# Optimization experiments

Hardware: AMD Instinct MI355X
Metric: run time of the kernel (lower is better)

Reference implementation:

```python
import jax, jax.numpy as jnp
import numpy as np

ALPHA = 3.0      # sharpness in tanh(alpha * lin(x)) (HypergraphConstructor)
TOPK = 10        # scale_hyperedges: neighbors per node in similarity topk
NEG_SLOPE = 0.2  # LeakyReLU slope in HypergraphAttention


def setup_inputs() -> dict:
    key = jax.random.key(0)
    ks = jax.random.split(key, 8)
    B, L, N, F, D, E = 16, 64, 512, 64, 64, 40
    return {
        "x": jax.random.normal(ks[0], (B, L, N, F), jnp.float32),
        "idx": jnp.arange(N, dtype=jnp.int64) if jax.config.jax_enable_x64 else jnp.arange(N, dtype=jnp.int32),
        "emb1": 0.1 * jax.random.normal(ks[1], (N, E), jnp.float32),
        "lin1_w": jax.random.normal(ks[2], (E, E), jnp.float32) / np.float32(np.sqrt(E)),
        "lin1_b": jnp.zeros((E,), jnp.float32),
        "W_self": 0.1 * jax.random.normal(ks[3], (F, D), jnp.float32),
        "W_neigh": 0.1 * jax.random.normal(ks[4], (F, D), jnp.float32),
        "W_concat": 0.1 * jax.random.normal(ks[5], (2 * D, D), jnp.float32),
        "attention": 0.1 * jax.random.normal(ks[6], (2 * D, 1), jnp.float32),
    }


def build_incidence(idx, emb1, lin1_w, lin1_b):
    """HypergraphConstructor (similarity-topk branch). Returns H: (N_nodes, M_hyperedges)."""
    feats = jnp.tanh(ALPHA * (emb1[idx] @ lin1_w + lin1_b))        # (N, E)
    sim = feats @ feats.T                                          # (N, N)
    _, top = jax.lax.top_k(sim, TOPK)                              # (N, k) indices
    n = feats.shape[0]
    rows = jnp.arange(n)[:, None]
    H = jnp.zeros((n, n), feats.dtype).at[rows, top].set(1.0)      # row i = hyperedge from node i's neighbors
    return H.T                                                     # (N nodes, M hyperedges)


def hypergraph_attention(x, H, W_self, W_neigh, W_concat, attention):
    """Faithful HypergraphAttention.forward (eval mode: dropout is identity)."""
    x_self = jnp.einsum('blnf,fd->blnd', x, W_self)
    # aggregate nodes -> hyperedges: H.T[m,n] == H[n,m]
    he = jnp.einsum('nm,blnf->blmf', H, x)                          # (B, L, M, F)
    e_deg = jnp.maximum(H.sum(axis=0), 1.0)                        # (M,)
    he = he / e_deg[None, None, :, None]
    he = jnp.where(he >= 0, he, NEG_SLOPE * he)                    # LeakyReLU(0.2)
    # scatter hyperedges -> nodes
    x_neigh = jnp.einsum('nm,blmf->blnf', H, he)                   # (B, L, N, F)
    n_deg = jnp.maximum(H.sum(axis=1), 1.0)                        # (N,)
    x_neigh = x_neigh / n_deg[None, None, :, None]
    x_neigh = jnp.einsum('blnf,fd->blnd', x_neigh, W_neigh)
    x_cat = jnp.concatenate([x_self, x_neigh], axis=-1)            # (B, L, N, 2D)
    scores = jnp.squeeze(x_cat @ attention, axis=-1)               # (B, L, N)
    w = jax.nn.softmax(scores, axis=-1)                            # softmax over nodes
    return (x_cat * w[..., None]) @ W_concat                       # (B, L, N, D)


def reference(x, idx, emb1, lin1_w, lin1_b, W_self, W_neigh, W_concat, attention):
    H = build_incidence(idx, emb1, lin1_w, lin1_b)
    return hypergraph_attention(x, H, W_self, W_neigh, W_concat, attention)
```

## Files before the change

kernel.cpp:

```cpp
#include <hip/hip_runtime.h>

#define N_NODES 512
#define E_DIM   40
#define TOPK    10

typedef unsigned short u16;
typedef __attribute__((ext_vector_type(8))) short short8;
typedef __attribute__((ext_vector_type(4))) float f32x4;

__device__ __forceinline__ u16 f2bf(float f) {
    unsigned int b = __float_as_uint(f);
    b += 0x7fffu + ((b >> 16) & 1u);
    return (u16)(b >> 16);
}
__device__ __forceinline__ float bf2f(u16 u) {
    return __uint_as_float(((unsigned int)u) << 16);
}
__device__ __forceinline__ unsigned pk2(float a, float b) {
    return (unsigned)f2bf(a) | ((unsigned)f2bf(b) << 16);
}

__global__ void prep_kernel(const float* __restrict__ emb1,
                            const float* __restrict__ w,
                            const float* __restrict__ b,
                            float* __restrict__ feats,
                            const float* __restrict__ Ws, const float* __restrict__ Wn,
                            const float* __restrict__ Wc, const float* __restrict__ att,
                            u16* __restrict__ Wt, float* __restrict__ ap) {
    if (blockIdx.x < N_NODES) {
        int n = blockIdx.x, e = threadIdx.x;
        if (e >= E_DIM) return;
        const float* er = emb1 + n * E_DIM;
        float s = b[e];
        for (int k = 0; k < E_DIM; ++k) s += er[k] * w[k * E_DIM + e];
        feats[n * E_DIM + e] = tanhf(3.0f * s);
    } else {
        int f = blockIdx.x - N_NODES, d = threadIdx.x;
        float a = 0.f, bb = 0.f;
        for (int k = 0; k < 64; ++k) {
            a  += Ws[f * 64 + k] * Wc[k * 64 + d];
            bb += Wn[f * 64 + k] * Wc[(64 + k) * 64 + d];
        }
        Wt[d * 128 + f]      = f2bf(a);
        Wt[d * 128 + 64 + f] = f2bf(bb);
        float p0 = Ws[f * 64 + d] * att[d];
        float p1 = Wn[f * 64 + d] * att[64 + d];
        for (int off = 32; off > 0; off >>= 1) {
            p0 += __shfl_down(p0, off);
            p1 += __shfl_down(p1, off);
        }
        if (d == 0) { ap[f] = p0; ap[64 + f] = p1; }
    }
}

#define TOPK_SMEM (512 * 41 * 4 + 4 * 512 * 4)

__global__ __launch_bounds__(256) void topk_kernel(const float* __restrict__ feats,
                                                   u16* __restrict__ top16) {
    extern __shared__ float tsm[];
    float* sf   = tsm;
    float* ssim = tsm + 512 * 41;
    const int tid = threadIdx.x;
    for (int i = tid; i < 512 * E_DIM; i += 256) {
        int n = i / E_DIM, k = i - n * E_DIM;
        sf[n * 41 + k] = feats[i];
    }
    __syncthreads();
    const int wv = tid >> 6, lane = tid & 63;
    const int m = blockIdx.x * 4 + wv;
    float* sim = ssim + wv * 512;

    float fm[E_DIM];
#pragma unroll
    for (int k = 0; k < E_DIM; ++k) fm[k] = sf[m * 41 + k];
    for (int n = lane; n < N_NODES; n += 64) {
        const float* fr = &sf[n * 41];
        float s = 0.f;
#pragma unroll
        for (int k = 0; k < E_DIM; ++k) s += fm[k] * fr[k];
        sim[n] = s;
    }
    __syncthreads();
    for (int it = 0; it < TOPK; ++it) {
        float bv = -3.0e38f; int bi = 1 << 30;
        for (int n = lane; n < N_NODES; n += 64) {
            float v = sim[n];
            if (v > bv) { bv = v; bi = n; }
        }
        for (int off = 32; off > 0; off >>= 1) {
            float ov = __shfl_down(bv, off);
            int   oi = __shfl_down(bi, off);
            if (ov > bv || (ov == bv && oi < bi)) { bv = ov; bi = oi; }
        }
        bi = __shfl(bi, 0);
        if (lane == 0) top16[m * 16 + it] = (u16)bi;
        __syncthreads();
        sim[bi] = -3.0e38f;
        __syncthreads();
    }
}

__global__ void hbuild_kernel(const u16* __restrict__ top16,
                              u16* __restrict__ Hrow, u16* __restrict__ H,
                              int* __restrict__ deg) {
    int m = threadIdx.x;
#pragma unroll
    for (int j = 0; j < TOPK; ++j) {
        int n = (int)top16[m * 16 + j];
        Hrow[m * 512 + n] = 0x3F80;
        H[n * 512 + m]    = 0x3F80;
        atomicAdd(&deg[n], 1);
    }
}

#define SC_OFF  65536
#define RED_OFF 67584
#define SMEM_BYTES 67648

__device__ __forceinline__ int t64_byte(int f, int g) {
    return f * 1024 + ((g ^ (f & 7)) << 4);
}
__device__ __forceinline__ int rm_byte(int n, int g) {
    return n * 128 + ((g ^ (n & 7)) << 4);
}

__global__ __launch_bounds__(256, 2) void main_kernel(
    const float* __restrict__ x,
    const u16* __restrict__ Hrow, const u16* __restrict__ H,
    const int* __restrict__ deg,
    const u16* __restrict__ Wt, const float* __restrict__ ap,
    float* __restrict__ out)
{
    extern __shared__ char smem[];
    float* sc  = (float*)(smem + SC_OFF);
    float* red = (float*)(smem + RED_OFF);

    const int bl  = blockIdx.x;
    const int tid = threadIdx.x;
    const int wv = tid >> 6, lane = tid & 63;
    const int lrow = lane & 15, lk = lane >> 4;
    const float* xr   = x   + (size_t)bl * N_NODES * 64;
    float*       outr = out + (size_t)bl * N_NODES * 64;

    float sv2[2];
#pragma unroll
    for (int r = 0; r < 2; ++r) {
        const int row = tid + r * 256;
        const float4* px = (const float4*)(xr + row * 64);
        const int gcol = row >> 3, bcol = (row & 7) * 2;
        float s = 0.f;
#pragma unroll
        for (int g = 0; g < 8; ++g) {
            float4 v0 = px[2 * g], v1 = px[2 * g + 1];
            float4 a0 = *(const float4*)(ap + g * 8);
            float4 a1 = *(const float4*)(ap + g * 8 + 4);
            s += v0.x * a0.x + v0.y * a0.y + v0.z * a0.z + v0.w * a0.w
               + v1.x * a1.x + v1.y * a1.y + v1.z * a1.z + v1.w * a1.w;
            float vf[8] = { v0.x, v0.y, v0.z, v0.w, v1.x, v1.y, v1.z, v1.w };
#pragma unroll
            for (int j = 0; j < 8; ++j) {
                int f = g * 8 + j;
                *(u16*)(smem + t64_byte(f, gcol) + bcol) = f2bf(vf[j]);
            }
        }
        sv2[r] = s;
    }
    __syncthreads();

    {
        f32x4 acc[2][4][4];
#pragma unroll
        for (int h = 0; h < 2; ++h)
#pragma unroll
            for (int mt = 0; mt < 4; ++mt)
#pragma unroll
                for (int ft = 0; ft < 4; ++ft) acc[h][mt][ft] = (f32x4)0.f;
        for (int ks = 0; ks < 16; ++ks) {
            short8 bfr[4];
#pragma unroll
            for (int ft = 0; ft < 4; ++ft)
                bfr[ft] = *(const short8*)(smem + t64_byte(ft * 16 + lrow, ks * 4 + lk));
#pragma unroll
            for (int h = 0; h < 2; ++h) {
                const int wveff = wv + 4 * h;
                short8 afr[4];
#pragma unroll
                for (int mt = 0; mt < 4; ++mt)
                    afr[mt] = *(const short8*)(Hrow + (wveff * 64 + mt * 16 + lrow) * 512
                                                    + ks * 32 + lk * 8);
#pragma unroll
                for (int mt = 0; mt < 4; ++mt)
#pragma unroll
                    for (int ft = 0; ft < 4; ++ft)
                        acc[h][mt][ft] = __builtin_amdgcn_mfma_f32_16x16x32_bf16(
                            afr[mt], bfr[ft], acc[h][mt][ft], 0, 0, 0);
            }
        }
        __syncthreads();
#pragma unroll
        for (int h = 0; h < 2; ++h) {
            const int wveff = wv + 4 * h;
#pragma unroll
            for (int mt = 0; mt < 4; ++mt) {
                const int gm = wveff * 8 + mt * 2 + (lk >> 1);
#pragma unroll
                for (int ft = 0; ft < 4; ++ft) {
                    const int f = ft * 16 + lrow;
                    float v[4];
#pragma unroll
                    for (int r = 0; r < 4; ++r) {
                        float t = acc[h][mt][ft][r] * 0.1f;
                        v[r] = t >= 0.f ? t : 0.2f * t;
                    }
                    *(uint2*)(smem + t64_byte(f, gm) + (lk & 1) * 8) =
                        make_uint2(pk2(v[0], v[1]), pk2(v[2], v[3]));
                }
            }
        }
    }
    __syncthreads();

    {
        f32x4 acc[2][4][4];
#pragma unroll
        for (int h = 0; h < 2; ++h)
#pragma unroll
            for (int nt = 0; nt < 4; ++nt)
#pragma unroll
                for (int ft = 0; ft < 4; ++ft) acc[h][nt][ft] = (f32x4)0.f;
        for (int ks = 0; ks < 16; ++ks) {
            short8 afr[4];
#pragma unroll
            for (int ft = 0; ft < 4; ++ft)
                afr[ft] = *(const short8*)(smem + t64_byte(ft * 16 + lrow, ks * 4 + lk));
#pragma unroll
            for (int h = 0; h < 2; ++h) {
                const int wveff = wv + 4 * h;
                short8 bfr[4];
#pragma unroll
                for (int nt = 0; nt < 4; ++nt)
                    bfr[nt] = *(const short8*)(H + (wveff * 64 + nt * 16 + lrow) * 512
                                                 + ks * 32 + lk * 8);
#pragma unroll
                for (int nt = 0; nt < 4; ++nt)
#pragma unroll
                    for (int ft = 0; ft < 4; ++ft)
                        acc[h][nt][ft] = __builtin_amdgcn_mfma_f32_16x16x32_bf16(
                            afr[ft], bfr[nt], acc[h][nt][ft], 0, 0, 0);
            }
        }
        __syncthreads();
#pragma unroll
        for (int h = 0; h < 2; ++h) {
#pragma unroll
            for (int nt = 0; nt < 4; ++nt) {
                const int n = (wv + 4 * h) * 64 + nt * 16 + lrow;
                int dg = deg[n];
                const float ideg = 1.0f / (float)(dg > 0 ? dg : 1);
#pragma unroll
                for (int ft = 0; ft < 4; ++ft) {
                    const int gf = ft * 2 + (lk >> 1);
                    *(uint2*)(smem + rm_byte(n, gf) + (lk & 1) * 8) =
                        make_uint2(pk2(acc[h][nt][ft][0] * ideg, acc[h][nt][ft][1] * ideg),
                                   pk2(acc[h][nt][ft][2] * ideg, acc[h][nt][ft][3] * ideg));
                }
            }
        }
    }
    __syncthreads();

#pragma unroll
    for (int r = 0; r < 2; ++r) {
        const int row = tid + r * 256;
        float s = sv2[r];
#pragma unroll
        for (int g = 0; g < 8; ++g) {
            short8 q = *(const short8*)(smem + rm_byte(row, g));
            float4 b0 = *(const float4*)(ap + 64 + g * 8);
            float4 b1 = *(const float4*)(ap + 64 + g * 8 + 4);
            s += bf2f((u16)q[0]) * b0.x + bf2f((u16)q[1]) * b0.y
               + bf2f((u16)q[2]) * b0.z + bf2f((u16)q[3]) * b0.w
               + bf2f((u16)q[4]) * b1.x + bf2f((u16)q[5]) * b1.y
               + bf2f((u16)q[6]) * b1.z + bf2f((u16)q[7]) * b1.w;
        }
        sv2[r] = s;
    }
    float bv = fmaxf(sv2[0], sv2[1]);
#pragma unroll
    for (int off = 32; off > 0; off >>= 1) bv = fmaxf(bv, __shfl_xor(bv, off));
    if (lane == 0) red[wv] = bv;
    __syncthreads();
    float M = fmaxf(fmaxf(red[0], red[1]), fmaxf(red[2], red[3]));
    float e0 = expf(sv2[0] - M), e1 = expf(sv2[1] - M);
    sc[tid] = e0;
    sc[tid + 256] = e1;
    float sv = e0 + e1;
#pragma unroll
    for (int off = 32; off > 0; off >>= 1) sv += __shfl_xor(sv, off);
    if (lane == 0) red[4 + wv] = sv;
    __syncthreads();
    const float invS = 1.0f / (red[4] + red[5] + red[6] + red[7]);

#pragma unroll 1
    for (int h = 0; h < 2; ++h) {
        const int wveff = wv + 4 * h;
        for (int nt = 0; nt < 4; ++nt) {
            const int n = wveff * 64 + nt * 16 + lrow;
            f32x4 accn[4];
#pragma unroll
            for (int dt = 0; dt < 4; ++dt) accn[dt] = (f32x4)0.f;
#pragma unroll
            for (int ks = 0; ks < 4; ++ks) {
                short8 bfrag;
                if (ks < 2) {
                    const float4* px = (const float4*)(xr + n * 64 + ks * 32 + lk * 8);
                    float4 v0 = px[0], v1 = px[1];
                    union { uint4 u; short8 s8; } cv;
                    cv.u.x = pk2(v0.x, v0.y); cv.u.y = pk2(v0.z, v0.w);
                    cv.u.z = pk2(v1.x, v1.y); cv.u.w = pk2(v1.z, v1.w);
                    bfrag = cv.s8;
                } else {
                    int gx = (ks - 2) * 4 + lk;
                    bfrag = *(const short8*)(smem + rm_byte(n, gx));
                }
#pragma unroll
                for (int dt = 0; dt < 4; ++dt) {
                    short8 wfrag = *(const short8*)(Wt + (dt * 16 + lrow) * 128
                                                       + ks * 32 + lk * 8);
                    accn[dt] = __builtin_amdgcn_mfma_f32_16x16x32_bf16(
                        wfrag, bfrag, accn[dt], 0, 0, 0);
                }
            }
            const float ww = sc[n] * invS;
#pragma unroll
            for (int dt = 0; dt < 4; ++dt) {
                float4 f;
                f.x = accn[dt][0] * ww; f.y = accn[dt][1] * ww;
                f.z = accn[dt][2] * ww; f.w = accn[dt][3] * ww;
                *(float4*)(outr + n * 64 + dt * 16 + lk * 4) = f;
            }
        }
    }
}

#define WS_FEATS 0
#define WS_TOP   81920
#define WS_WT    98304
#define WS_AP    114688
#define WS_DEG   115200
#define WS_HROW  131072
#define WS_H     655360
#define WS_END   1179648

extern "C" void kernel_launch(void* const* d_in, const int* in_sizes, int n_in,
                              void* d_out, int out_size, void* d_ws, size_t ws_size,
                              hipStream_t stream) {
    const float* x        = (const float*)d_in[0];
    const float* emb1     = (const float*)d_in[2];
    const float* lin1_w   = (const float*)d_in[3];
    const float* lin1_b   = (const float*)d_in[4];
    const float* W_self   = (const float*)d_in[5];
    const float* W_neigh  = (const float*)d_in[6];
    const float* W_concat = (const float*)d_in[7];
    const float* att      = (const float*)d_in[8];
    float* out = (float*)d_out;

    char* ws = (char*)d_ws;
    float* feats = (float*)(ws + WS_FEATS);
    u16*   top16 = (u16*)  (ws + WS_TOP);
    u16*   Wt    = (u16*)  (ws + WS_WT);
    float* ap    = (float*)(ws + WS_AP);
    int*   deg   = (int*)  (ws + WS_DEG);
    u16*   Hrow  = (u16*)  (ws + WS_HROW);
    u16*   H     = (u16*)  (ws + WS_H);

    prep_kernel<<<N_NODES + 64, 64, 0, stream>>>(emb1, lin1_w, lin1_b, feats,
                                                 W_self, W_neigh, W_concat, att, Wt, ap);

    (void)hipFuncSetAttribute((const void*)topk_kernel,
                              hipFuncAttributeMaxDynamicSharedMemorySize, TOPK_SMEM);
    topk_kernel<<<128, 256, TOPK_SMEM, stream>>>(feats, top16);

    (void)hipMemsetAsync(ws + WS_DEG, 0, WS_END - WS_DEG, stream);
    hbuild_kernel<<<1, 512, 0, stream>>>(top16, Hrow, H, deg);

    (void)hipFuncSetAttribute((const void*)main_kernel,
                              hipFuncAttributeMaxDynamicSharedMemorySize, SMEM_BYTES);
    main_kernel<<<1024, 256, SMEM_BYTES, stream>>>(x, Hrow, H, deg, Wt, ap, out);
}
```

Before: 229.4 us.

## Split fused main kernel into hyperedge, softmax and output kernels for more parallelism

Replaces the single per-slice fused kernel with three kernels when the workspace is large enough. A hyperedge kernel computes the bf16 hyperedge features over 4096 blocks, and the attention term is folded algebraically so softmax scores come from x·a_self plus H·(he·a) per node. A separate softmax kernel computes the weights, and an output kernel over 2048 blocks does the scatter and final projection. This buys more blocks and higher occupancy (3 blocks per CU) at the cost of a 64MB heT round trip through memory plus extra launches. It also hardcodes the edge degree as 0.1, i.e. 1/TOPK, and uses atomics for hv.

```diff
diff --git a/kernel.cpp b/kernel.cpp
--- a/kernel.cpp
+++ b/kernel.cpp
@@ -113,15 +113,282 @@
     }
 }
 
+
+#define HE_SMEM 32832
+__device__ __forceinline__ int t32_byte(int f, int g) {
+    return f * 1024 + ((g ^ (f & 7)) << 4);
+}
+
+__global__ __launch_bounds__(256, 3) void he_kernel(
+    const float* __restrict__ x, const u16* __restrict__ Hrow,
+    const float* __restrict__ ap,
+    u16* __restrict__ heT, float* __restrict__ hv)
+{
+    extern __shared__ char smem[];
+    const int bid = blockIdx.x;
+    const int slice = bid >> 2, mhalf = (bid >> 1) & 1, fhalf = bid & 1;
+    const int tid = threadIdx.x;
+    const int wv = tid >> 6, lane = tid & 63;
+    const int lrow = lane & 15, lk = lane >> 4;
+    const float* xr = x + (size_t)slice * N_NODES * 64;
+    const int mbase = mhalf * 256 + wv * 64;
+
+#pragma unroll
+    for (int r = 0; r < 2; ++r) {
+        const int row = tid + r * 256;
+        const float4* px = (const float4*)(xr + row * 64 + fhalf * 32);
+        const int gcol = row >> 3, bcol = (row & 7) * 2;
+#pragma unroll
+        for (int g = 0; g < 4; ++g) {
+            float4 v0 = px[2 * g], v1 = px[2 * g + 1];
+            float vf[8] = { v0.x, v0.y, v0.z, v0.w, v1.x, v1.y, v1.z, v1.w };
+#pragma unroll
+            for (int j = 0; j < 8; ++j) {
+                int f = g * 8 + j;
+                *(u16*)(smem + t32_byte(f, gcol) + bcol) = f2bf(vf[j]);
+            }
+        }
+    }
+    __syncthreads();
+
+    f32x4 acc[4][2];
+#pragma unroll
+    for (int mt = 0; mt < 4; ++mt)
+#pragma unroll
+        for (int fh = 0; fh < 2; ++fh) acc[mt][fh] = (f32x4)0.f;
+    for (int ks = 0; ks < 16; ++ks) {
+        short8 afr[4], bfr[2];
+#pragma unroll
+        for (int mt = 0; mt < 4; ++mt)
+            afr[mt] = *(const short8*)(Hrow + (mbase + mt * 16 + lrow) * 512
+                                            + ks * 32 + lk * 8);
+#pragma unroll
+        for (int fh = 0; fh < 2; ++fh)
+            bfr[fh] = *(const short8*)(smem + t32_byte(fh * 16 + lrow, ks * 4 + lk));
+#pragma unroll
+        for (int mt = 0; mt < 4; ++mt)
+#pragma unroll
+            for (int fh = 0; fh < 2; ++fh)
+                acc[mt][fh] = __builtin_amdgcn_mfma_f32_16x16x32_bf16(
+                    afr[mt], bfr[fh], acc[mt][fh], 0, 0, 0);
+    }
+
+    float lv[4][2][4];
+#pragma unroll
+    for (int mt = 0; mt < 4; ++mt)
+#pragma unroll
+        for (int fh = 0; fh < 2; ++fh)
+#pragma unroll
+            for (int r = 0; r < 4; ++r) {
+                float t = acc[mt][fh][r] * 0.1f;
+                lv[mt][fh][r] = t >= 0.f ? t : 0.2f * t;
+            }
+
+#pragma unroll
+    for (int mt = 0; mt < 4; ++mt)
+#pragma unroll
+        for (int r = 0; r < 4; ++r) {
+            float p = lv[mt][0][r] * ap[64 + fhalf * 32 + lrow]
+                    + lv[mt][1][r] * ap[64 + fhalf * 32 + 16 + lrow];
+            p += __shfl_xor(p, 1);
+            p += __shfl_xor(p, 2);
+            p += __shfl_xor(p, 4);
+            p += __shfl_xor(p, 8);
+            if (lrow == 0)
+                atomicAdd(&hv[slice * 512 + mbase + mt * 16 + lk * 4 + r], p);
+        }
+    __syncthreads();
+
+#pragma unroll
+    for (int mt = 0; mt < 4; ++mt)
+#pragma unroll
+        for (int fh = 0; fh < 2; ++fh)
+#pragma unroll
+            for (int r = 0; r < 4; ++r) {
+                int f_l = fh * 16 + lrow;
+                int m_l = mt * 16 + lk * 4 + r;
+                *(u16*)(smem + wv * 4096 + f_l * 128
+                        + (((m_l >> 3) ^ (f_l & 7)) << 4) + (m_l & 7) * 2)
+                    = f2bf(lv[mt][fh][r]);
+            }
+    __syncthreads();
+
+    {
+        const int f_l = lane & 31, gb = (lane >> 5) * 4;
+#pragma unroll
+        for (int gi = 0; gi < 4; ++gi) {
+            int g = gb + gi;
+            uint4 v = *(const uint4*)(smem + wv * 4096 + f_l * 128
+                                      + ((g ^ (f_l & 7)) << 4));
+            *(uint4*)(heT + (size_t)slice * 32768 + (fhalf * 32 + f_l) * 512
+                      + mbase + g * 8) = v;
+        }
+    }
+}
+
+__global__ __launch_bounds__(512) void sm_kernel(
+    const float* __restrict__ x, const u16* __restrict__ H,
+    const int* __restrict__ deg, const float* __restrict__ ap,
+    const float* __restrict__ hv, float* __restrict__ wexp)
+{
+    __shared__ float hvl[512];
+    __shared__ float red[16];
+    const int slice = blockIdx.x, n = threadIdx.x;
+    const int wv = n >> 6, lane = n & 63;
+    hvl[n] = hv[slice * 512 + n];
+    __syncthreads();
+
+    const float4* px = (const float4*)(x + (size_t)slice * N_NODES * 64 + n * 64);
+    float s = 0.f;
+#pragma unroll
+    for (int g = 0; g < 8; ++g) {
+        float4 v0 = px[2 * g], v1 = px[2 * g + 1];
+        float4 a0 = *(const float4*)(ap + g * 8);
+        float4 a1 = *(const float4*)(ap + g * 8 + 4);
+        s += v0.x * a0.x + v0.y * a0.y + v0.z * a0.z + v0.w * a0.w
+           + v1.x * a1.x + v1.y * a1.y + v1.z * a1.z + v1.w * a1.w;
+    }
+    const uint4* hp = (const uint4*)(H + n * 512);
+    float t = 0.f;
+    for (int c = 0; c < 64; ++c) {
+        uint4 h = hp[c];
+        unsigned wd[4] = { h.x, h.y, h.z, h.w };
+#pragma unroll
+        for (int p = 0; p < 4; ++p) {
+            t += bf2f((u16)(wd[p] & 0xffff))  * hvl[c * 8 + p * 2];
+            t += bf2f((u16)(wd[p] >> 16))     * hvl[c * 8 + p * 2 + 1];
+        }
+    }
+    int dg = deg[n];
+    s += t * (1.0f / (float)(dg > 0 ? dg : 1));
+
+    float bv = s;
+#pragma unroll
+    for (int off = 32; off > 0; off >>= 1) bv = fmaxf(bv, __shfl_xor(bv, off));
+    if (lane == 0) red[wv] = bv;
+    __syncthreads();
+    float M = red[0];
+#pragma unroll
+    for (int w = 1; w < 8; ++w) M = fmaxf(M, red[w]);
+    float ev = expf(s - M);
+    float sv = ev;
+#pragma unroll
+    for (int off = 32; off > 0; off >>= 1) sv += __shfl_xor(sv, off);
+    if (lane == 0) red[8 + wv] = sv;
+    __syncthreads();
+    float S = red[8];
+#pragma unroll
+    for (int w = 1; w < 8; ++w) S += red[8 + w];
+    wexp[slice * 512 + n] = ev * (1.0f / S);
+}
+
+#define OUT_SMEM 32832
+__device__ __forceinline__ int rm_byte(int nl, int g) {
+    return nl * 128 + ((g ^ (nl & 7)) << 4);
+}
+
+__global__ __launch_bounds__(256, 3) void out_kernel(
+    const float* __restrict__ x, const u16* __restrict__ H,
+    const int* __restrict__ deg, const u16* __restrict__ heT,
+    const u16* __restrict__ Wt, const float* __restrict__ wexp,
+    float* __restrict__ out)
+{
+    extern __shared__ char smem[];
+    const int bid = blockIdx.x;
+    const int slice = bid >> 1, nhalf = bid & 1;
+    const int tid = threadIdx.x;
+    const int wv = tid >> 6, lane = tid & 63;
+    const int lrow = lane & 15, lk = lane >> 4;
+    const float* xr   = x   + (size_t)slice * N_NODES * 64;
+    float*       outr = out + (size_t)slice * N_NODES * 64;
+    const u16* heTs = heT + (size_t)slice * 32768;
+    const int nbase = nhalf * 256 + wv * 64;
+
+    {
+        f32x4 acc[4][4];
+#pragma unroll
+        for (int nt = 0; nt < 4; ++nt)
+#pragma unroll
+            for (int ft = 0; ft < 4; ++ft) acc[nt][ft] = (f32x4)0.f;
+        for (int ks = 0; ks < 16; ++ks) {
+            short8 afr[4], bfr[4];
+#pragma unroll
+            for (int ft = 0; ft < 4; ++ft)
+                afr[ft] = *(const short8*)(heTs + (ft * 16 + lrow) * 512
+                                                + ks * 32 + lk * 8);
+#pragma unroll
+            for (int nt = 0; nt < 4; ++nt)
+                bfr[nt] = *(const short8*)(H + (nbase + nt * 16 + lrow) * 512
+                                             + ks * 32 + lk * 8);
+#pragma unroll
+            for (int nt = 0; nt < 4; ++nt)
+#pragma unroll
+                for (int ft = 0; ft < 4; ++ft)
+                    acc[nt][ft] = __builtin_amdgcn_mfma_f32_16x16x32_bf16(
+                        afr[ft], bfr[nt], acc[nt][ft], 0, 0, 0);
+        }
+#pragma unroll
+        for (int nt = 0; nt < 4; ++nt) {
+            const int n = nbase + nt * 16 + lrow;
+            const int nl = n - nhalf * 256;
+            int dg = deg[n];
+            const float ideg = 1.0f / (float)(dg > 0 ? dg : 1);
+#pragma unroll
+            for (int ft = 0; ft < 4; ++ft) {
+                const int gf = ft * 2 + (lk >> 1);
+                *(uint2*)(smem + rm_byte(nl, gf) + (lk & 1) * 8) =
+                    make_uint2(pk2(acc[nt][ft][0] * ideg, acc[nt][ft][1] * ideg),
+                               pk2(acc[nt][ft][2] * ideg, acc[nt][ft][3] * ideg));
+            }
+        }
+    }
+    __syncthreads();
+
+    for (int nt = 0; nt < 4; ++nt) {
+        const int n = nbase + nt * 16 + lrow;
+        const int nl = n - nhalf * 256;
+        f32x4 accn[4];
+#pragma unroll
+        for (int dt = 0; dt < 4; ++dt) accn[dt] = (f32x4)0.f;
+#pragma unroll
+        for (int ks = 0; ks < 4; ++ks) {
+            short8 bfrag;
+            if (ks < 2) {
+                const float4* px = (const float4*)(xr + n * 64 + ks * 32 + lk * 8);
+                float4 v0 = px[0], v1 = px[1];
+                union { uint4 u; short8 s8; } cv;
+                cv.u.x = pk2(v0.x, v0.y); cv.u.y = pk2(v0.z, v0.w);
+                cv.u.z = pk2(v1.x, v1.y); cv.u.w = pk2(v1.z, v1.w);
+                bfrag = cv.s8;
+            } else {
+                int gx = (ks - 2) * 4 + lk;
+                bfrag = *(const short8*)(smem + rm_byte(nl, gx));
+            }
+#pragma unroll
+            for (int dt = 0; dt < 4; ++dt) {
+                short8 wfrag = *(const short8*)(Wt + (dt * 16 + lrow) * 128
+                                                   + ks * 32 + lk * 8);
+                accn[dt] = __builtin_amdgcn_mfma_f32_16x16x32_bf16(
+                    wfrag, bfrag, accn[dt], 0, 0, 0);
+            }
+        }
+        const float ww = wexp[slice * 512 + n];
+#pragma unroll
+        for (int dt = 0; dt < 4; ++dt) {
+            float4 f;
+            f.x = accn[dt][0] * ww; f.y = accn[dt][1] * ww;
+            f.z = accn[dt][2] * ww; f.w = accn[dt][3] * ww;
+            *(float4*)(outr + n * 64 + dt * 16 + lk * 4) = f;
+        }
+    }
+}
+
 #define SC_OFF  65536
 #define RED_OFF 67584
 #define SMEM_BYTES 67648
 
 __device__ __forceinline__ int t64_byte(int f, int g) {
     return f * 1024 + ((g ^ (f & 7)) << 4);
-}
-__device__ __forceinline__ int rm_byte(int n, int g) {
-    return n * 128 + ((g ^ (n & 7)) << 4);
 }
 
 __global__ __launch_bounds__(256, 2) void main_kernel(
@@ -343,14 +610,21 @@
     }
 }
 
-#define WS_FEATS 0
-#define WS_TOP   81920
-#define WS_WT    98304
-#define WS_AP    114688
-#define WS_DEG   115200
-#define WS_HROW  131072
-#define WS_H     655360
-#define WS_END   1179648
+#define WP_FEATS 0
+#define WP_TOP   81920
+#define WP_WT    98304
+#define WP_AP    114688
+#define WP_DEG   115200
+#define WP_HV    117248
+#define WP_HROW  2214400
+#define WP_H     2738688
+#define WP_WEXP  3262976
+#define WP_HET   5360128
+#define WP_END   (5360128 + 67108864)
+#define WF_DEG   115200
+#define WF_HROW  131072
+#define WF_H     655360
+#define WF_END   1179648
 
 extern "C" void kernel_launch(void* const* d_in, const int* in_sizes, int n_in,
                               void* d_out, int out_size, void* d_ws, size_t ws_size,
@@ -364,27 +638,56 @@
     const float* W_concat = (const float*)d_in[7];
     const float* att      = (const float*)d_in[8];
     float* out = (float*)d_out;
-
     char* ws = (char*)d_ws;
-    float* feats = (float*)(ws + WS_FEATS);
-    u16*   top16 = (u16*)  (ws + WS_TOP);
-    u16*   Wt    = (u16*)  (ws + WS_WT);
-    float* ap    = (float*)(ws + WS_AP);
-    int*   deg   = (int*)  (ws + WS_DEG);
-    u16*   Hrow  = (u16*)  (ws + WS_HROW);
-    u16*   H     = (u16*)  (ws + WS_H);
-
-    prep_kernel<<<N_NODES + 64, 64, 0, stream>>>(emb1, lin1_w, lin1_b, feats,
-                                                 W_self, W_neigh, W_concat, att, Wt, ap);
-
-    (void)hipFuncSetAttribute((const void*)topk_kernel,
-                              hipFuncAttributeMaxDynamicSharedMemorySize, TOPK_SMEM);
-    topk_kernel<<<128, 256, TOPK_SMEM, stream>>>(feats, top16);
-
-    (void)hipMemsetAsync(ws + WS_DEG, 0, WS_END - WS_DEG, stream);
-    hbuild_kernel<<<1, 512, 0, stream>>>(top16, Hrow, H, deg);
-
-    (void)hipFuncSetAttribute((const void*)main_kernel,
-                              hipFuncAttributeMaxDynamicSharedMemorySize, SMEM_BYTES);
-    main_kernel<<<1024, 256, SMEM_BYTES, stream>>>(x, Hrow, H, deg, Wt, ap, out);
-}
+
+    if (ws_size >= (size_t)WP_END) {
+        float* feats = (float*)(ws + WP_FEATS);
+        u16*   top16 = (u16*)  (ws + WP_TOP);
+        u16*   Wt    = (u16*)  (ws + WP_WT);
+        float* ap    = (float*)(ws + WP_AP);
+        int*   deg   = (int*)  (ws + WP_DEG);
+        float* hv    = (float*)(ws + WP_HV);
+        u16*   Hrow  = (u16*)  (ws + WP_HROW);
+        u16*   H     = (u16*)  (ws + WP_H);
+        float* wexp  = (float*)(ws + WP_WEXP);
+        u16*   heT   = (u16*)  (ws + WP_HET);
+
+        prep_kernel<<<N_NODES + 64, 64, 0, stream>>>(emb1, lin1_w, lin1_b, feats,
+                                                     W_self, W_neigh, W_concat, att,
+                                                     Wt, ap);
+        (void)hipFuncSetAttribute((const void*)topk_kernel,
+                                  hipFuncAttributeMaxDynamicSharedMemorySize, TOPK_SMEM);
+        topk_kernel<<<128, 256, TOPK_SMEM, stream>>>(feats, top16);
+        (void)hipMemsetAsync(ws + WP_DEG, 0, WP_WEXP - WP_DEG, stream);
+        hbuild_kernel<<<1, 512, 0, stream>>>(top16, Hrow, H, deg);
+
+        (void)hipFuncSetAttribute((const void*)he_kernel,
+                                  hipFuncAttributeMaxDynamicSharedMemorySize, HE_SMEM);
+        he_kernel<<<4096, 256, HE_SMEM, stream>>>(x, Hrow, ap, heT, hv);
+        sm_kernel<<<1024, 512, 0, stream>>>(x, H, deg, ap, hv, wexp);
+        (void)hipFuncSetAttribute((const void*)out_kernel,
+                                  hipFuncAttributeMaxDynamicSharedMemorySize, OUT_SMEM);
+        out_kernel<<<2048, 256, OUT_SMEM, stream>>>(x, H, deg, heT, Wt, wexp, out);
+    } else {
+        float* feats = (float*)(ws + WP_FEATS);
+        u16*   top16 = (u16*)  (ws + WP_TOP);
+        u16*   Wt    = (u16*)  (ws + WP_WT);
+        float* ap    = (float*)(ws + WP_AP);
+        int*   deg   = (int*)  (ws + WF_DEG);
+        u16*   Hrow  = (u16*)  (ws + WF_HROW);
+        u16*   H     = (u16*)  (ws + WF_H);
+
+        prep_kernel<<<N_NODES + 64, 64, 0, stream>>>(emb1, lin1_w, lin1_b, feats,
+                                                     W_self, W_neigh, W_concat, att,
+                                                     Wt, ap);
+        (void)hipFuncSetAttribute((const void*)topk_kernel,
+                                  hipFuncAttributeMaxDynamicSharedMemorySize, TOPK_SMEM);
+        topk_kernel<<<128, 256, TOPK_SMEM, stream>>>(feats, top16);
+        (void)hipMemsetAsync(ws + WF_DEG, 0, WF_END - WF_DEG, stream);
+        hbuild_kernel<<<1, 512, 0, stream>>>(top16, Hrow, H, deg);
+
+        (void)hipFuncSetAttribute((const void*)main_kernel,
+                                  hipFuncAttributeMaxDynamicSharedMemorySize, SMEM_BYTES);
+        main_kernel<<<1024, 256, SMEM_BYTES, stream>>>(x, Hrow, H, deg, Wt, ap, out);
+    }
+}
```

New measurement: 482.1 us. 2.1x slower.
